# Performance work log

Hardware: AMD Instinct MI355X
Metric: run time of the kernel (lower is better)

## Reference

```python
import jax, jax.numpy as jnp
import numpy as np
from jax import lax

CHANS = [3, 4, 8, 16, 32, 64, 128]


def _conv_relu(x, w, b):
    # x: [B,Cin,H,W], w: [Cout,Cin,4,4], stride 2, pad 1
    y = lax.conv_general_dilated(x, w, (2, 2), [(1, 1), (1, 1)],
                                 dimension_numbers=('NCHW', 'OIHW', 'NCHW'))
    return jax.nn.relu(y + b[None, :, None, None])


def setup_inputs() -> dict:
    key = jax.random.key(0)
    ks = jax.random.split(key, 64)
    T, B, S = 3, 2048, 64
    d = {"img_seq": jax.random.normal(ks[0], (T, B, 3, S, S), jnp.float32)}
    i = 1
    for l in range(6):
        cin, cout = CHANS[l], CHANS[l + 1]
        d[f"enc_w{l}"] = jax.random.normal(ks[i], (T, cout, cin, 4, 4), jnp.float32) / np.sqrt(cin * 16); i += 1
        d[f"enc_b{l}"] = jnp.zeros((T, cout), jnp.float32)
    # MLP 128 -> 32 -> 32 -> 64
    d["mlp_w1"] = jax.random.normal(ks[i], (32, 128), jnp.float32) / np.sqrt(128.0); i += 1
    d["mlp_b1"] = jnp.zeros((32,), jnp.float32)
    d["mlp_w2"] = jax.random.normal(ks[i], (32, 32), jnp.float32) / np.sqrt(32.0); i += 1
    d["mlp_b2"] = jnp.zeros((32,), jnp.float32)
    d["mlp_w3"] = jax.random.normal(ks[i], (64, 32), jnp.float32) / np.sqrt(32.0); i += 1
    d["mlp_b3"] = jnp.zeros((64,), jnp.float32)
    # LSTM: input 64, hidden 20 (torch gate order i,f,g,o)
    H = 20
    d["w_ih"] = jax.random.normal(ks[i], (4 * H, 64), jnp.float32) / np.sqrt(64.0); i += 1
    d["w_hh"] = jax.random.normal(ks[i], (4 * H, H), jnp.float32) / np.sqrt(float(H)); i += 1
    d["b_ih"] = jnp.zeros((4 * H,), jnp.float32)
    d["b_hh"] = jnp.zeros((4 * H,), jnp.float32)
    # 20 reward heads: 20 -> 32 -> 32 -> 1, stacked on leading K axis
    K = 20
    d["head_w1"] = jax.random.normal(ks[i], (K, 32, H), jnp.float32) / np.sqrt(float(H)); i += 1
    d["head_b1"] = jnp.zeros((K, 32), jnp.float32)
    d["head_w2"] = jax.random.normal(ks[i], (K, 32, 32), jnp.float32) / np.sqrt(32.0); i += 1
    d["head_b2"] = jnp.zeros((K, 32), jnp.float32)
    d["head_w3"] = jax.random.normal(ks[i], (K, 1, 32), jnp.float32) / np.sqrt(32.0); i += 1
    d["head_b3"] = jnp.zeros((K, 1), jnp.float32)
    return d


def reference(img_seq,
              enc_w0, enc_b0, enc_w1, enc_b1, enc_w2, enc_b2,
              enc_w3, enc_b3, enc_w4, enc_b4, enc_w5, enc_b5,
              mlp_w1, mlp_b1, mlp_w2, mlp_b2, mlp_w3, mlp_b3,
              w_ih, w_hh, b_ih, b_hh,
              head_w1, head_b1, head_w2, head_b2, head_w3, head_b3):
    # Per-frame CNN encoders (one encoder per time step) -> vmap over T
    def encode(img, w0, b0, w1, b1, w2, b2, w3, b3, w4, b4, w5, b5):
        x = _conv_relu(img, w0, b0)
        x = _conv_relu(x, w1, b1)
        x = _conv_relu(x, w2, b2)
        x = _conv_relu(x, w3, b3)
        x = _conv_relu(x, w4, b4)
        x = _conv_relu(x, w5, b5)  # [B,128,1,1]
        return x.reshape(x.shape[0], -1)  # [B,128]

    enc = jax.vmap(encode)(img_seq, enc_w0, enc_b0, enc_w1, enc_b1, enc_w2, enc_b2,
                           enc_w3, enc_b3, enc_w4, enc_b4, enc_w5, enc_b5)  # [T,B,128]

    # Shared MLP 128 -> 64
    h = jax.nn.relu(jnp.einsum('tbd,od->tbo', enc, mlp_w1) + mlp_b1)
    h = jax.nn.relu(jnp.einsum('tbd,od->tbo', h, mlp_w2) + mlp_b2)
    feats = jnp.einsum('tbd,od->tbo', h, mlp_w3) + mlp_b3  # [T,B,64]

    # Single-layer LSTM over T
    B, H = feats.shape[1], w_hh.shape[1]
    def step(carry, x_t):
        hs, cs = carry
        gates = x_t @ w_ih.T + hs @ w_hh.T + b_ih + b_hh  # [B,4H]
        i, f, g, o = jnp.split(gates, 4, axis=-1)
        cs = jax.nn.sigmoid(f) * cs + jax.nn.sigmoid(i) * jnp.tanh(g)
        hs = jax.nn.sigmoid(o) * jnp.tanh(cs)
        return (hs, cs), hs
    init = (jnp.zeros((B, H), feats.dtype), jnp.zeros((B, H), feats.dtype))
    _, h_seq = lax.scan(step, init, feats)  # [T,B,20]

    # 20 reward heads applied to every LSTM output, batched over head axis k
    x1 = jax.nn.relu(jnp.einsum('tbd,kod->ktbo', h_seq, head_w1) + head_b1[:, None, None, :])
    x2 = jax.nn.relu(jnp.einsum('ktbd,kod->ktbo', x1, head_w2) + head_b2[:, None, None, :])
    out = jnp.einsum('ktbd,kod->ktbo', x2, head_w3) + head_b3[:, None, None, :]  # [20,T,B,1]
    return out
```

## Files before the change

### kernel.cpp

```cpp
#include <hip/hip_runtime.h>
#include <math.h>

#define T_DIM 3
#define B_DIM 2048
#define NIMG  (T_DIM * B_DIM)

__global__ __launch_bounds__(256) void conv0_kernel(
    const float* __restrict__ img, const float* __restrict__ w0,
    const float* __restrict__ b0, float* __restrict__ a0)
{
    __shared__ float sb[2][64 * 68];

    const int bid  = blockIdx.x;
    const int ohp  = bid & 15;
    const int g    = (bid >> 4) & 31;
    const int t    = bid >> 9;
    const int tid  = threadIdx.x;
    const int wv   = tid >> 6;
    const int lane = tid & 63;
    const int oh_sub = wv >> 1;
    const int half   = wv & 1;
    const int oh   = ohp * 2 + oh_sub;
    const int ow0  = half * 16;
    const int im   = g * 64 + lane;

    const int jj16 = tid >> 4;
    const int f4   = tid & 15;
    const int ih0  = 4 * ohp - 1;

    float acc[4][16];
#pragma unroll
    for (int j = 0; j < 4; j++) {
        const float bv = b0[t * 4 + j];
#pragma unroll
        for (int k = 0; k < 16; k++) acc[j][k] = bv;
    }
    const float* wt = w0 + t * 192;

    auto stage = [&](int ci, int ih, float* dst) {
        if ((unsigned)ih < 64u) {
#pragma unroll
            for (int p = 0; p < 4; ++p) {
                const int j = p * 16 + jj16;
                const float4 v = *(const float4*)(img +
                    ((size_t)((t * 2048 + g * 64 + j) * 3 + ci) << 12) +
                    (ih << 6) + (f4 << 2));
                *(float4*)&dst[j * 68 + (f4 << 2)] = v;
            }
        }
    };

    auto consume = [&](int ci, int r, int ih, const float* src) {
        const int kh = r - 2 * oh_sub;
        if (kh < 0 || kh > 3 || (unsigned)ih >= 64u) return;
        const float* lrow = src + lane * 68;
        float tap[34];
        if (half == 0) {
            tap[0] = 0.f;
#pragma unroll
            for (int c = 0; c < 8; ++c) {
                const float4 v = *(const float4*)(lrow + 4 * c);
                tap[1 + 4 * c] = v.x; tap[2 + 4 * c] = v.y;
                tap[3 + 4 * c] = v.z; tap[4 + 4 * c] = v.w;
            }
            tap[33] = lrow[32];
        } else {
            tap[0] = lrow[31];
#pragma unroll
            for (int c = 0; c < 8; ++c) {
                const float4 v = *(const float4*)(lrow + 32 + 4 * c);
                tap[1 + 4 * c] = v.x; tap[2 + 4 * c] = v.y;
                tap[3 + 4 * c] = v.z; tap[4 + 4 * c] = v.w;
            }
            tap[33] = 0.f;
        }
        float w_[4][4];
#pragma unroll
        for (int j = 0; j < 4; j++)
#pragma unroll
            for (int kw = 0; kw < 4; kw++)
                w_[j][kw] = wt[((j * 3 + ci) * 4 + kh) * 4 + kw];
#pragma unroll
        for (int jj = 0; jj < 16; jj++)
#pragma unroll
            for (int kw = 0; kw < 4; kw++) {
                const float x = tap[2 * jj + kw];
#pragma unroll
                for (int j = 0; j < 4; j++)
                    acc[j][jj] = fmaf(x, w_[j][kw], acc[j][jj]);
            }
    };

    stage(0, ih0, sb[0]);
    __syncthreads();
    int s = 0;
#pragma unroll
    for (int ci = 0; ci < 3; ++ci)
#pragma unroll
        for (int r = 0; r < 6; ++r) {
            if (s < 17) {
                const int rn = (r == 5) ? 0 : r + 1;
                const int cn = (r == 5) ? ci + 1 : ci;
                stage(cn, ih0 + rn, sb[(s + 1) & 1]);
            }
            consume(ci, r, ih0 + r, sb[s & 1]);
            __syncthreads();
            ++s;
        }

    const size_t ob0 = ((size_t)(t * 4096 + oh * 32 + ow0)) * 2048 + im;
#pragma unroll
    for (int j = 0; j < 4; j++)
#pragma unroll
        for (int k = 0; k < 16; k++)
            a0[ob0 + ((size_t)j * 1024 + k) * 2048] = fmaxf(acc[j][k], 0.f);
}

template<int CIN, int COUT, int IH, int OH, int CB>
__device__ __forceinline__ void convmid(
    const float* __restrict__ in, const float* __restrict__ gw,
    const float* __restrict__ gb, float* __restrict__ out,
    int t, int cg, int oh, int im)
{
    const int co0 = cg * CB;
    float acc[CB][OH];
#pragma unroll
    for (int j = 0; j < CB; j++) {
        const float bv = gb[t * COUT + co0 + j];
#pragma unroll
        for (int k = 0; k < OH; k++) acc[j][k] = bv;
    }
    const float* wt = gw + ((size_t)t * COUT + co0) * CIN * 16;
    const size_t inb = ((size_t)t * CIN) * (IH * IH) * 2048 + im;

#pragma unroll 4
    for (int ci = 0; ci < CIN; ci++) {
#pragma unroll
        for (int kh = 0; kh < 4; kh++) {
            const int ih = 2 * oh - 1 + kh;
            if ((unsigned)ih >= (unsigned)IH) continue;
            const float* rp = in + inb + (size_t)(ci * IH + ih) * IH * 2048;
            float tap[IH + 2];
            tap[0] = 0.f; tap[IH + 1] = 0.f;
#pragma unroll
            for (int iw = 0; iw < IH; iw++) tap[iw + 1] = rp[(size_t)iw * 2048];
            float w_[CB][4];
#pragma unroll
            for (int j = 0; j < CB; j++)
#pragma unroll
                for (int kw = 0; kw < 4; kw++)
                    w_[j][kw] = wt[((size_t)j * CIN + ci) * 16 + kh * 4 + kw];
#pragma unroll
            for (int ow = 0; ow < OH; ow++)
#pragma unroll
                for (int kw = 0; kw < 4; kw++) {
                    const float x = tap[2 * ow + kw];
#pragma unroll
                    for (int j = 0; j < CB; j++)
                        acc[j][ow] = fmaf(x, w_[j][kw], acc[j][ow]);
                }
        }
    }
    const size_t ob = ((size_t)(t * COUT + co0) * OH * OH + (size_t)oh * OH) * 2048 + im;
#pragma unroll
    for (int j = 0; j < CB; j++)
#pragma unroll
        for (int k = 0; k < OH; k++)
            out[ob + ((size_t)j * OH * OH + k) * 2048] = fmaxf(acc[j][k], 0.f);
}

__global__ __launch_bounds__(256) void conv1_kernel(
    const float* __restrict__ a0, const float* __restrict__ w,
    const float* __restrict__ b, float* __restrict__ a1)
{
    const int wid = blockIdx.x * 4 + (threadIdx.x >> 6);
    const int lane = threadIdx.x & 63;
    const int oh = wid & 15, cg = (wid >> 4) & 1, g = (wid >> 5) & 31, t = wid >> 10;
    convmid<4, 8, 32, 16, 4>(a0, w, b, a1, t, cg, oh, g * 64 + lane);
}

__global__ __launch_bounds__(256) void conv2_kernel(
    const float* __restrict__ a1, const float* __restrict__ w,
    const float* __restrict__ b, float* __restrict__ a2)
{
    const int wid = blockIdx.x * 4 + (threadIdx.x >> 6);
    const int lane = threadIdx.x & 63;
    const int oh = wid & 7, cg = (wid >> 3) & 3, g = (wid >> 5) & 31, t = wid >> 10;
    convmid<8, 16, 16, 8, 4>(a1, w, b, a2, t, cg, oh, g * 64 + lane);
}

__global__ __launch_bounds__(256) void conv3_kernel(
    const float* __restrict__ a2, const float* __restrict__ w,
    const float* __restrict__ b, float* __restrict__ a3)
{
    const int wid = blockIdx.x * 4 + (threadIdx.x >> 6);
    const int lane = threadIdx.x & 63;
    const int oh = wid & 3, cg = (wid >> 2) & 3, g = (wid >> 4) & 31, t = wid >> 9;
    convmid<16, 32, 8, 4, 8>(a2, w, b, a3, t, cg, oh, g * 64 + lane);
}

__global__ __launch_bounds__(256) void conv4_kernel(
    const float* __restrict__ a3, const float* __restrict__ w4,
    const float* __restrict__ b4, float* __restrict__ a4)
{
    const int wid = blockIdx.x * 4 + (threadIdx.x >> 6);
    const int lane = threadIdx.x & 63;
    const int cg = wid & 15, g = (wid >> 4) & 31, t = wid >> 9;
    const int im = g * 64 + lane;
    const int co0 = cg * 4;

    float acc[4][4];
#pragma unroll
    for (int j = 0; j < 4; j++) {
        const float bv = b4[t * 64 + co0 + j];
#pragma unroll
        for (int p = 0; p < 4; p++) acc[j][p] = bv;
    }
    const float* wt = w4 + ((size_t)t * 64 + co0) * 32 * 16;
    const size_t inb = ((size_t)t * 32) * 16 * 2048 + im;

    for (int ci = 0; ci < 32; ci++) {
        float tin[16];
#pragma unroll
        for (int p = 0; p < 16; p++)
            tin[p] = a3[inb + ((size_t)ci * 16 + p) * 2048];
#pragma unroll
        for (int kh = 0; kh < 4; kh++)
#pragma unroll
            for (int oh = 0; oh < 2; oh++) {
                const int ih = 2 * oh - 1 + kh;
                if (ih < 0 || ih > 3) continue;
#pragma unroll
                for (int ow = 0; ow < 2; ow++)
#pragma unroll
                    for (int kw = 0; kw < 4; kw++) {
                        const int iw = 2 * ow - 1 + kw;
                        if (iw < 0 || iw > 3) continue;
                        const float x = tin[ih * 4 + iw];
#pragma unroll
                        for (int j = 0; j < 4; j++)
                            acc[j][oh * 2 + ow] = fmaf(
                                x, wt[((size_t)j * 32 + ci) * 16 + kh * 4 + kw],
                                acc[j][oh * 2 + ow]);
                    }
            }
    }
#pragma unroll
    for (int j = 0; j < 4; j++)
#pragma unroll
        for (int p = 0; p < 4; p++)
            a4[(((size_t)t * 64 + co0 + j) * 4 + p) * 2048 + im] =
                fmaxf(acc[j][p], 0.f);
}

__global__ __launch_bounds__(256) void conv5_kernel(
    const float* __restrict__ a4, const float* __restrict__ w5,
    const float* __restrict__ b5, float* __restrict__ feats)
{
    const int wid = blockIdx.x * 4 + (threadIdx.x >> 6);
    const int lane = threadIdx.x & 63;
    const int cg = wid & 31, g = (wid >> 5) & 31, t = wid >> 10;
    const int im = g * 64 + lane;
    const int co0 = cg * 4;

    float acc[4];
#pragma unroll
    for (int j = 0; j < 4; j++) acc[j] = b5[t * 128 + co0 + j];
    const float* wt = w5 + ((size_t)t * 128 + co0) * 64 * 16;
    const size_t inb = ((size_t)t * 64) * 4 * 2048 + im;

#pragma unroll 4
    for (int ci = 0; ci < 64; ci++) {
        const float x0 = a4[inb + ((size_t)ci * 4 + 0) * 2048];
        const float x1 = a4[inb + ((size_t)ci * 4 + 1) * 2048];
        const float x2 = a4[inb + ((size_t)ci * 4 + 2) * 2048];
        const float x3 = a4[inb + ((size_t)ci * 4 + 3) * 2048];
#pragma unroll
        for (int j = 0; j < 4; j++) {
            const size_t wb = ((size_t)j * 64 + ci) * 16;
            acc[j] = fmaf(x0, wt[wb + 5],  acc[j]);
            acc[j] = fmaf(x1, wt[wb + 6],  acc[j]);
            acc[j] = fmaf(x2, wt[wb + 9],  acc[j]);
            acc[j] = fmaf(x3, wt[wb + 10], acc[j]);
        }
    }
#pragma unroll
    for (int j = 0; j < 4; j++)
        feats[((size_t)t * 128 + co0 + j) * 2048 + im] = fmaxf(acc[j], 0.f);
}


__global__ __launch_bounds__(64, 1) void mlpxg_kernel(
    const float* __restrict__ feats,
    const float* __restrict__ mw1, const float* __restrict__ mb1,
    const float* __restrict__ mw2, const float* __restrict__ mb2,
    const float* __restrict__ mw3, const float* __restrict__ mb3,
    const float* __restrict__ wih, const float* __restrict__ bih,
    const float* __restrict__ bhh, float* __restrict__ xg)
{
    const int tb = blockIdx.x;
    const int t  = tb >> 5, bg = tb & 31;
    const int b  = bg * 64 + threadIdx.x;

    float x[128];
#pragma unroll
    for (int d = 0; d < 128; ++d)
        x[d] = feats[((size_t)t * 128 + d) * 2048 + b];

    float h1[32];
#pragma unroll
    for (int o = 0; o < 32; ++o) {
        float a = mb1[o];
        const float4* wr = (const float4*)(mw1 + o * 128);
#pragma unroll
        for (int q = 0; q < 32; ++q) {
            const float4 w = wr[q];
            a = fmaf(w.x, x[4 * q + 0], a); a = fmaf(w.y, x[4 * q + 1], a);
            a = fmaf(w.z, x[4 * q + 2], a); a = fmaf(w.w, x[4 * q + 3], a);
        }
        h1[o] = fmaxf(a, 0.f);
    }
    float h2[32];
#pragma unroll
    for (int o = 0; o < 32; ++o) {
        float a = mb2[o];
        const float4* wr = (const float4*)(mw2 + o * 32);
#pragma unroll
        for (int q = 0; q < 8; ++q) {
            const float4 w = wr[q];
            a = fmaf(w.x, h1[4 * q + 0], a); a = fmaf(w.y, h1[4 * q + 1], a);
            a = fmaf(w.z, h1[4 * q + 2], a); a = fmaf(w.w, h1[4 * q + 3], a);
        }
        h2[o] = fmaxf(a, 0.f);
    }
    float f_[64];
#pragma unroll
    for (int o = 0; o < 64; ++o) {
        float a = mb3[o];
        const float4* wr = (const float4*)(mw3 + o * 32);
#pragma unroll
        for (int q = 0; q < 8; ++q) {
            const float4 w = wr[q];
            a = fmaf(w.x, h2[4 * q + 0], a); a = fmaf(w.y, h2[4 * q + 1], a);
            a = fmaf(w.z, h2[4 * q + 2], a); a = fmaf(w.w, h2[4 * q + 3], a);
        }
        f_[o] = a;
    }
#pragma unroll
    for (int i = 0; i < 80; ++i) {
        float a = bih[i] + bhh[i];
        const float4* wr = (const float4*)(wih + i * 64);
#pragma unroll
        for (int q = 0; q < 16; ++q) {
            const float4 w = wr[q];
            a = fmaf(w.x, f_[4 * q + 0], a); a = fmaf(w.y, f_[4 * q + 1], a);
            a = fmaf(w.z, f_[4 * q + 2], a); a = fmaf(w.w, f_[4 * q + 3], a);
        }
        xg[((size_t)t * 80 + i) * 2048 + b] = a;
    }
}

__global__ __launch_bounds__(64, 1) void lstm_kernel(
    const float* __restrict__ xg, const float* __restrict__ whh,
    float* __restrict__ hseq)
{
    const int b = blockIdx.x * 64 + threadIdx.x;
    float h[20], c[20];
#pragma unroll
    for (int j = 0; j < 20; ++j) { h[j] = 0.f; c[j] = 0.f; }

    for (int t = 0; t < 3; ++t) {
        float gv[80];
#pragma unroll
        for (int i = 0; i < 80; ++i) {
            float a = xg[((size_t)t * 80 + i) * 2048 + b];
            const float4* wr = (const float4*)(whh + i * 20);
#pragma unroll
            for (int q = 0; q < 5; ++q) {
                const float4 w = wr[q];
                a = fmaf(w.x, h[4 * q + 0], a); a = fmaf(w.y, h[4 * q + 1], a);
                a = fmaf(w.z, h[4 * q + 2], a); a = fmaf(w.w, h[4 * q + 3], a);
            }
            gv[i] = a;
        }
#pragma unroll
        for (int j = 0; j < 20; ++j) {
            const float ig = 1.f / (1.f + expf(-gv[j]));
            const float fg = 1.f / (1.f + expf(-gv[20 + j]));
            const float gt = tanhf(gv[40 + j]);
            const float og = 1.f / (1.f + expf(-gv[60 + j]));
            const float cn = fg * c[j] + ig * gt;
            c[j] = cn;
            const float hn = og * tanhf(cn);
            h[j] = hn;
            hseq[((size_t)t * 20 + j) * 2048 + b] = hn;
        }
    }
}

__global__ __launch_bounds__(64, 1) void heads_kernel(
    const float* __restrict__ hseq,
    const float* __restrict__ hw1, const float* __restrict__ hb1,
    const float* __restrict__ hw2, const float* __restrict__ hb2,
    const float* __restrict__ hw3, const float* __restrict__ hb3,
    float* __restrict__ out)
{
    const int t  = blockIdx.x >> 5, bg = blockIdx.x & 31;
    const int k  = blockIdx.y;
    const int b  = bg * 64 + threadIdx.x;

    float xv[20];
#pragma unroll
    for (int d = 0; d < 20; ++d)
        xv[d] = hseq[((size_t)t * 20 + d) * 2048 + b];

    float a1[32];
#pragma unroll
    for (int o = 0; o < 32; ++o) {
        float a = hb1[k * 32 + o];
        const float4* wr = (const float4*)(hw1 + ((size_t)k * 32 + o) * 20);
#pragma unroll
        for (int q = 0; q < 5; ++q) {
            const float4 w = wr[q];
            a = fmaf(w.x, xv[4 * q + 0], a); a = fmaf(w.y, xv[4 * q + 1], a);
            a = fmaf(w.z, xv[4 * q + 2], a); a = fmaf(w.w, xv[4 * q + 3], a);
        }
        a1[o] = fmaxf(a, 0.f);
    }
    float a2[32];
#pragma unroll
    for (int o = 0; o < 32; ++o) {
        float a = hb2[k * 32 + o];
        const float4* wr = (const float4*)(hw2 + ((size_t)k * 32 + o) * 32);
#pragma unroll
        for (int q = 0; q < 8; ++q) {
            const float4 w = wr[q];
            a = fmaf(w.x, a1[4 * q + 0], a); a = fmaf(w.y, a1[4 * q + 1], a);
            a = fmaf(w.z, a1[4 * q + 2], a); a = fmaf(w.w, a1[4 * q + 3], a);
        }
        a2[o] = fmaxf(a, 0.f);
    }
    float r = hb3[k];
    const float4* wr = (const float4*)(hw3 + (size_t)k * 32);
#pragma unroll
    for (int q = 0; q < 8; ++q) {
        const float4 w = wr[q];
        r = fmaf(w.x, a2[4 * q + 0], r); r = fmaf(w.y, a2[4 * q + 1], r);
        r = fmaf(w.z, a2[4 * q + 2], r); r = fmaf(w.w, a2[4 * q + 3], r);
    }
    out[((size_t)k * 3 + t) * 2048 + b] = r;
}

extern "C" void kernel_launch(void* const* d_in, const int* in_sizes, int n_in,
                              void* d_out, int out_size, void* d_ws, size_t ws_size,
                              hipStream_t stream)
{
    const float* img = (const float*)d_in[0];
    const float* ew0 = (const float*)d_in[1];  const float* eb0 = (const float*)d_in[2];
    const float* ew1 = (const float*)d_in[3];  const float* eb1 = (const float*)d_in[4];
    const float* ew2 = (const float*)d_in[5];  const float* eb2 = (const float*)d_in[6];
    const float* ew3 = (const float*)d_in[7];  const float* eb3 = (const float*)d_in[8];
    const float* ew4 = (const float*)d_in[9];  const float* eb4 = (const float*)d_in[10];
    const float* ew5 = (const float*)d_in[11]; const float* eb5 = (const float*)d_in[12];
    const float* mw1 = (const float*)d_in[13]; const float* mb1 = (const float*)d_in[14];
    const float* mw2 = (const float*)d_in[15]; const float* mb2 = (const float*)d_in[16];
    const float* mw3 = (const float*)d_in[17]; const float* mb3 = (const float*)d_in[18];
    const float* wih = (const float*)d_in[19]; const float* whh = (const float*)d_in[20];
    const float* bih = (const float*)d_in[21]; const float* bhh = (const float*)d_in[22];
    const float* hw1 = (const float*)d_in[23]; const float* hb1 = (const float*)d_in[24];
    const float* hw2 = (const float*)d_in[25]; const float* hb2 = (const float*)d_in[26];
    const float* hw3 = (const float*)d_in[27]; const float* hb3 = (const float*)d_in[28];

    float* A  = (float*)d_ws;
    float* B  = A + 25165824;
    float* C  = B + 12582912;
    float* XG = B;
    float* HS = B + 491520;

    conv0_kernel<<<1536, 256, 0, stream>>>(img, ew0, eb0, A);
    conv1_kernel<<< 768, 256, 0, stream>>>(A, ew1, eb1, B);
    conv2_kernel<<< 768, 256, 0, stream>>>(B, ew2, eb2, A);
    conv3_kernel<<< 384, 256, 0, stream>>>(A, ew3, eb3, B);
    conv4_kernel<<< 384, 256, 0, stream>>>(B, ew4, eb4, A);
    conv5_kernel<<< 768, 256, 0, stream>>>(A, ew5, eb5, C);
    mlpxg_kernel<<<96, 64, 0, stream>>>(C, mw1, mb1, mw2, mb2, mw3, mb3,
                                        wih, bih, bhh, XG);
    lstm_kernel<<<32, 64, 0, stream>>>(XG, whh, HS);
    heads_kernel<<<dim3(96, 20), 64, 0, stream>>>(HS, hw1, hb1, hw2, hb2,
                                                  hw3, hb3, (float*)d_out);
}
```

Before: 1.079 ms.

## Fold mlp_w3 into LSTM input weights and restream MLP/LSTM loops to cut registers

Adds a small kernel that precomputes W_ih·mlp_w3 and the combined bias, so the MLP's last linear layer and the LSTM input projection become one 32-to-80 matvec. The first MLP layer now streams input features four at a time instead of holding all 128 in registers. The LSTM step computes its four gates per hidden unit on the fly rather than building an 80-entry gate array. The heads kernel swaps float4 weight loads for scalar loads. The goal is to cut FLOPs and register pressure in the tiny post-conv kernels, at the cost of one extra launch and slightly different rounding from the reassociated matmul.

After: 1.002 ms. 1.08x faster.

```diff
diff --git a/kernel.cpp b/kernel.cpp
--- a/kernel.cpp
+++ b/kernel.cpp
@@ -290,73 +290,76 @@
 }
 
 
+__global__ __launch_bounds__(256) void fusew_kernel(
+    const float* __restrict__ wih, const float* __restrict__ mw3,
+    const float* __restrict__ mb3, const float* __restrict__ bih,
+    const float* __restrict__ bhh, float* __restrict__ WX,
+    float* __restrict__ BX)
+{
+    const int idx = blockIdx.x * 256 + threadIdx.x;
+    if (idx < 2560) {
+        const int i = idx >> 5, d = idx & 31;
+        float a = 0.f;
+        for (int o = 0; o < 64; ++o)
+            a = fmaf(wih[i * 64 + o], mw3[o * 32 + d], a);
+        WX[idx] = a;
+    } else if (idx < 2640) {
+        const int i = idx - 2560;
+        float a = bih[i] + bhh[i];
+        for (int o = 0; o < 64; ++o)
+            a = fmaf(wih[i * 64 + o], mb3[o], a);
+        BX[i] = a;
+    }
+}
+
 __global__ __launch_bounds__(64, 1) void mlpxg_kernel(
     const float* __restrict__ feats,
     const float* __restrict__ mw1, const float* __restrict__ mb1,
     const float* __restrict__ mw2, const float* __restrict__ mb2,
-    const float* __restrict__ mw3, const float* __restrict__ mb3,
-    const float* __restrict__ wih, const float* __restrict__ bih,
-    const float* __restrict__ bhh, float* __restrict__ xg)
-{
-    const int tb = blockIdx.x;
-    const int t  = tb >> 5, bg = tb & 31;
+    const float* __restrict__ WX,  const float* __restrict__ BX,
+    float* __restrict__ xg)
+{
+    const int t  = blockIdx.x >> 5, bg = blockIdx.x & 31;
     const int b  = bg * 64 + threadIdx.x;
 
-    float x[128];
-#pragma unroll
-    for (int d = 0; d < 128; ++d)
-        x[d] = feats[((size_t)t * 128 + d) * 2048 + b];
-
     float h1[32];
 #pragma unroll
-    for (int o = 0; o < 32; ++o) {
-        float a = mb1[o];
-        const float4* wr = (const float4*)(mw1 + o * 128);
-#pragma unroll
-        for (int q = 0; q < 32; ++q) {
-            const float4 w = wr[q];
-            a = fmaf(w.x, x[4 * q + 0], a); a = fmaf(w.y, x[4 * q + 1], a);
-            a = fmaf(w.z, x[4 * q + 2], a); a = fmaf(w.w, x[4 * q + 3], a);
-        }
-        h1[o] = fmaxf(a, 0.f);
-    }
+    for (int o = 0; o < 32; ++o) h1[o] = mb1[o];
+
+    const float* fb = feats + (size_t)t * 128 * 2048 + b;
+    for (int d4 = 0; d4 < 32; ++d4) {
+        const float x0 = fb[(size_t)(4 * d4 + 0) * 2048];
+        const float x1 = fb[(size_t)(4 * d4 + 1) * 2048];
+        const float x2 = fb[(size_t)(4 * d4 + 2) * 2048];
+        const float x3 = fb[(size_t)(4 * d4 + 3) * 2048];
+#pragma unroll
+        for (int o = 0; o < 32; ++o) {
+            const float4 w = *(const float4*)(mw1 + o * 128 + 4 * d4);
+            h1[o] = fmaf(w.w, x3, fmaf(w.z, x2, fmaf(w.y, x1,
+                    fmaf(w.x, x0, h1[o]))));
+        }
+    }
+#pragma unroll
+    for (int o = 0; o < 32; ++o) h1[o] = fmaxf(h1[o], 0.f);
+
     float h2[32];
 #pragma unroll
     for (int o = 0; o < 32; ++o) {
         float a = mb2[o];
-        const float4* wr = (const float4*)(mw2 + o * 32);
-#pragma unroll
-        for (int q = 0; q < 8; ++q) {
-            const float4 w = wr[q];
-            a = fmaf(w.x, h1[4 * q + 0], a); a = fmaf(w.y, h1[4 * q + 1], a);
-            a = fmaf(w.z, h1[4 * q + 2], a); a = fmaf(w.w, h1[4 * q + 3], a);
-        }
+#pragma unroll
+        for (int d = 0; d < 32; ++d)
+            a = fmaf(mw2[o * 32 + d], h1[d], a);
         h2[o] = fmaxf(a, 0.f);
     }
-    float f_[64];
-#pragma unroll
-    for (int o = 0; o < 64; ++o) {
-        float a = mb3[o];
-        const float4* wr = (const float4*)(mw3 + o * 32);
-#pragma unroll
-        for (int q = 0; q < 8; ++q) {
-            const float4 w = wr[q];
-            a = fmaf(w.x, h2[4 * q + 0], a); a = fmaf(w.y, h2[4 * q + 1], a);
-            a = fmaf(w.z, h2[4 * q + 2], a); a = fmaf(w.w, h2[4 * q + 3], a);
-        }
-        f_[o] = a;
-    }
-#pragma unroll
+
+    float* xb = xg + (size_t)t * 80 * 2048 + b;
+#pragma unroll 4
     for (int i = 0; i < 80; ++i) {
-        float a = bih[i] + bhh[i];
-        const float4* wr = (const float4*)(wih + i * 64);
-#pragma unroll
-        for (int q = 0; q < 16; ++q) {
-            const float4 w = wr[q];
-            a = fmaf(w.x, f_[4 * q + 0], a); a = fmaf(w.y, f_[4 * q + 1], a);
-            a = fmaf(w.z, f_[4 * q + 2], a); a = fmaf(w.w, f_[4 * q + 3], a);
-        }
-        xg[((size_t)t * 80 + i) * 2048 + b] = a;
+        float a = BX[i];
+#pragma unroll
+        for (int d = 0; d < 32; ++d)
+            a = fmaf(WX[i * 32 + d], h2[d], a);
+        xb[(size_t)i * 2048] = a;
     }
 }
 
@@ -370,31 +373,33 @@
     for (int j = 0; j < 20; ++j) { h[j] = 0.f; c[j] = 0.f; }
 
     for (int t = 0; t < 3; ++t) {
-        float gv[80];
-#pragma unroll
-        for (int i = 0; i < 80; ++i) {
-            float a = xg[((size_t)t * 80 + i) * 2048 + b];
-            const float4* wr = (const float4*)(whh + i * 20);
-#pragma unroll
-            for (int q = 0; q < 5; ++q) {
-                const float4 w = wr[q];
-                a = fmaf(w.x, h[4 * q + 0], a); a = fmaf(w.y, h[4 * q + 1], a);
-                a = fmaf(w.z, h[4 * q + 2], a); a = fmaf(w.w, h[4 * q + 3], a);
-            }
-            gv[i] = a;
-        }
+        const float* xb = xg + (size_t)t * 80 * 2048 + b;
+        float hn[20];
 #pragma unroll
         for (int j = 0; j < 20; ++j) {
-            const float ig = 1.f / (1.f + expf(-gv[j]));
-            const float fg = 1.f / (1.f + expf(-gv[20 + j]));
-            const float gt = tanhf(gv[40 + j]);
-            const float og = 1.f / (1.f + expf(-gv[60 + j]));
+            float ai = xb[(size_t)(j +  0) * 2048];
+            float af = xb[(size_t)(j + 20) * 2048];
+            float ag = xb[(size_t)(j + 40) * 2048];
+            float ao = xb[(size_t)(j + 60) * 2048];
+#pragma unroll
+            for (int d = 0; d < 20; ++d) {
+                const float hv = h[d];
+                ai = fmaf(whh[(j +  0) * 20 + d], hv, ai);
+                af = fmaf(whh[(j + 20) * 20 + d], hv, af);
+                ag = fmaf(whh[(j + 40) * 20 + d], hv, ag);
+                ao = fmaf(whh[(j + 60) * 20 + d], hv, ao);
+            }
+            const float ig = 1.f / (1.f + expf(-ai));
+            const float fg = 1.f / (1.f + expf(-af));
+            const float gt = tanhf(ag);
+            const float og = 1.f / (1.f + expf(-ao));
             const float cn = fg * c[j] + ig * gt;
-            c[j] = cn;
-            const float hn = og * tanhf(cn);
-            h[j] = hn;
-            hseq[((size_t)t * 20 + j) * 2048 + b] = hn;
-        }
+            c[j]  = cn;
+            hn[j] = og * tanhf(cn);
+            hseq[((size_t)t * 20 + j) * 2048 + b] = hn[j];
+        }
+#pragma unroll
+        for (int j = 0; j < 20; ++j) h[j] = hn[j];
     }
 }
 
@@ -418,36 +423,24 @@
 #pragma unroll
     for (int o = 0; o < 32; ++o) {
         float a = hb1[k * 32 + o];
-        const float4* wr = (const float4*)(hw1 + ((size_t)k * 32 + o) * 20);
-#pragma unroll
-        for (int q = 0; q < 5; ++q) {
-            const float4 w = wr[q];
-            a = fmaf(w.x, xv[4 * q + 0], a); a = fmaf(w.y, xv[4 * q + 1], a);
-            a = fmaf(w.z, xv[4 * q + 2], a); a = fmaf(w.w, xv[4 * q + 3], a);
-        }
+#pragma unroll
+        for (int d = 0; d < 20; ++d)
+            a = fmaf(hw1[((size_t)k * 32 + o) * 20 + d], xv[d], a);
         a1[o] = fmaxf(a, 0.f);
     }
     float a2[32];
 #pragma unroll
     for (int o = 0; o < 32; ++o) {
         float a = hb2[k * 32 + o];
-        const float4* wr = (const float4*)(hw2 + ((size_t)k * 32 + o) * 32);
-#pragma unroll
-        for (int q = 0; q < 8; ++q) {
-            const float4 w = wr[q];
-            a = fmaf(w.x, a1[4 * q + 0], a); a = fmaf(w.y, a1[4 * q + 1], a);
-            a = fmaf(w.z, a1[4 * q + 2], a); a = fmaf(w.w, a1[4 * q + 3], a);
-        }
+#pragma unroll
+        for (int d = 0; d < 32; ++d)
+            a = fmaf(hw2[((size_t)k * 32 + o) * 32 + d], a1[d], a);
         a2[o] = fmaxf(a, 0.f);
     }
     float r = hb3[k];
-    const float4* wr = (const float4*)(hw3 + (size_t)k * 32);
-#pragma unroll
-    for (int q = 0; q < 8; ++q) {
-        const float4 w = wr[q];
-        r = fmaf(w.x, a2[4 * q + 0], r); r = fmaf(w.y, a2[4 * q + 1], r);
-        r = fmaf(w.z, a2[4 * q + 2], r); r = fmaf(w.w, a2[4 * q + 3], r);
-    }
+#pragma unroll
+    for (int d = 0; d < 32; ++d)
+        r = fmaf(hw3[(size_t)k * 32 + d], a2[d], r);
     out[((size_t)k * 3 + t) * 2048 + b] = r;
 }
 
@@ -474,17 +467,20 @@
     float* A  = (float*)d_ws;
     float* B  = A + 25165824;
     float* C  = B + 12582912;
+    float* D  = C + 786432;
     float* XG = B;
     float* HS = B + 491520;
-
+    float* WX = D;
+    float* BX = D + 2560;
+
+    fusew_kernel<<<11, 256, 0, stream>>>(wih, mw3, mb3, bih, bhh, WX, BX);
     conv0_kernel<<<1536, 256, 0, stream>>>(img, ew0, eb0, A);
     conv1_kernel<<< 768, 256, 0, stream>>>(A, ew1, eb1, B);
     conv2_kernel<<< 768, 256, 0, stream>>>(B, ew2, eb2, A);
     conv3_kernel<<< 384, 256, 0, stream>>>(A, ew3, eb3, B);
     conv4_kernel<<< 384, 256, 0, stream>>>(B, ew4, eb4, A);
     conv5_kernel<<< 768, 256, 0, stream>>>(A, ew5, eb5, C);
-    mlpxg_kernel<<<96, 64, 0, stream>>>(C, mw1, mb1, mw2, mb2, mw3, mb3,
-                                        wih, bih, bhh, XG);
+    mlpxg_kernel<<<96, 64, 0, stream>>>(C, mw1, mb1, mw2, mb2, WX, BX, XG);
     lstm_kernel<<<32, 64, 0, stream>>>(XG, whh, HS);
     heads_kernel<<<dim3(96, 20), 64, 0, stream>>>(HS, hw1, hb1, hw2, hb2,
                                                   hw3, hb3, (float*)d_out);
```
